# Performance work log

Measured on AMD Instinct MI355X. Metric: run time of the kernel, lower is better.

## Reference

```python
import jax, jax.numpy as jnp
import numpy as np

NUM_FIELDS = 39
_ROW, _COL = np.triu_indices(NUM_FIELDS, k=1)  # 741 pairs, matches the double loop in __init__


def setup_inputs() -> dict:
    key = jax.random.key(0)
    x = jax.random.normal(key, (16384, NUM_FIELDS, 64), dtype=jnp.float32)
    return {"x": x}


def reference(x) -> jnp.ndarray:
    # Original: p=x[:,row,:,None], q=x[:,col,None,:], pq=p@q (B,P,d,d), then sum over both d axes.
    # sum_{a,b} p_a * q_b == (sum_a p_a) * (sum_b q_b), so we fuse and never build the d x d outer.
    s = jnp.sum(x, axis=-1)                     # [B, F] per-field embedding sums
    return s[:, _ROW] * s[:, _COL]              # [B, P] with P = F*(F-1)/2 = 741
```

## Files before the change

kernel.cpp:

```cpp
#include <hip/hip_runtime.h>

#define NF 39
#define NP 741

struct PairLUT { unsigned short rc[NP]; };

constexpr PairLUT make_lut() {
    PairLUT L{};
    int p = 0;
    for (int i = 0; i < NF; ++i)
        for (int j = i + 1; j < NF; ++j) {
            L.rc[p] = (unsigned short)((i << 8) | j);
            ++p;
        }
    return L;
}

__constant__ PairLUT LUT = make_lut();

__global__ __launch_bounds__(256) void opn_kernel(const float* __restrict__ x,
                                                  float* __restrict__ out) {
    const int b   = blockIdx.x;
    const int tid = threadIdx.x;
    __shared__ float s[NF + 1];

    const int g = tid >> 4;
    const int l = tid & 15;

    const float* xb = x + (size_t)b * (NF * 64);

    #pragma unroll
    for (int base = 0; base < NF; base += 16) {
        const int f = base + g;
        float v = 0.0f;
        if (f < NF) {
            const float4 t = *reinterpret_cast<const float4*>(xb + f * 64 + l * 4);
            v = (t.x + t.y) + (t.z + t.w);
        }
        v += __shfl_xor(v, 1);
        v += __shfl_xor(v, 2);
        v += __shfl_xor(v, 4);
        v += __shfl_xor(v, 8);
        if (f < NF && l == 0) s[f] = v;
    }
    __syncthreads();

    float* ob = out + (size_t)b * NP;
    #pragma unroll
    for (int p = tid; p < NP; p += 256) {
        const unsigned int rc = LUT.rc[p];
        ob[p] = s[rc >> 8] * s[rc & 255u];
    }
}

extern "C" void kernel_launch(void* const* d_in, const int* in_sizes, int n_in,
                              void* d_out, int out_size, void* d_ws, size_t ws_size,
                              hipStream_t stream) {
    const float* x = (const float*)d_in[0];
    float* out = (float*)d_out;
    const int B = in_sizes[0] / (NF * 64);
    opn_kernel<<<B, 256, 0, stream>>>(x, out);
}
```

Before: 37.74 us.

## Assign one wavefront per batch row and drop block-wide barrier

Each 64-lane wavefront now handles a whole batch row, with four rows per 256-thread block. All ten float4 loads per lane are issued up front before the shuffle reductions, and the block-wide __syncthreads is removed because each wave reads only its own shared-memory slice. Outputs are written with nontemporal stores. The grid is B/4, which assumes B is divisible by 4 and depends on the wave having finished its LDS writes before it reads them back without a barrier.

Result: no change. 37.28 us (median of 2 runs) (-1.2%).

```diff
diff --git a/kernel.cpp b/kernel.cpp
--- a/kernel.cpp
+++ b/kernel.cpp
@@ -2,6 +2,7 @@
 
 #define NF 39
 #define NP 741
+#define N4 624
 
 struct PairLUT { unsigned short rc[NP]; };
 
@@ -20,36 +21,46 @@
 
 __global__ __launch_bounds__(256) void opn_kernel(const float* __restrict__ x,
                                                   float* __restrict__ out) {
-    const int b   = blockIdx.x;
     const int tid = threadIdx.x;
-    __shared__ float s[NF + 1];
+    const int wid = tid >> 6;
+    const int l   = tid & 63;
+    const int b   = blockIdx.x * 4 + wid;
 
-    const int g = tid >> 4;
-    const int l = tid & 15;
+    __shared__ float s[4][NF + 1];
 
-    const float* xb = x + (size_t)b * (NF * 64);
+    const float4* xb4 = reinterpret_cast<const float4*>(x) + (size_t)b * N4;
+
+    float v[10];
+    #pragma unroll
+    for (int r = 0; r < 9; ++r) {
+        const float4 t = xb4[r * 64 + l];
+        v[r] = (t.x + t.y) + (t.z + t.w);
+    }
+    {
+        float4 t = {0.f, 0.f, 0.f, 0.f};
+        if (576 + l < N4) t = xb4[576 + l];
+        v[9] = (t.x + t.y) + (t.z + t.w);
+    }
 
     #pragma unroll
-    for (int base = 0; base < NF; base += 16) {
-        const int f = base + g;
-        float v = 0.0f;
-        if (f < NF) {
-            const float4 t = *reinterpret_cast<const float4*>(xb + f * 64 + l * 4);
-            v = (t.x + t.y) + (t.z + t.w);
-        }
-        v += __shfl_xor(v, 1);
-        v += __shfl_xor(v, 2);
-        v += __shfl_xor(v, 4);
-        v += __shfl_xor(v, 8);
-        if (f < NF && l == 0) s[f] = v;
+    for (int r = 0; r < 10; ++r) {
+        float vv = v[r];
+        vv += __shfl_xor(vv, 1);
+        vv += __shfl_xor(vv, 2);
+        vv += __shfl_xor(vv, 4);
+        vv += __shfl_xor(vv, 8);
+        const int f = r * 4 + (l >> 4);
+        if ((l & 15) == 0 && f < NF) s[wid][f] = vv;
     }
-    __syncthreads();
 
     float* ob = out + (size_t)b * NP;
     #pragma unroll
-    for (int p = tid; p < NP; p += 256) {
-        const unsigned int rc = LUT.rc[p];
-        ob[p] = s[rc >> 8] * s[rc & 255u];
+    for (int k = 0; k < 12; ++k) {
+        const int p = k * 64 + l;
+        if (p < NP) {
+            const unsigned int rc = LUT.rc[p];
+            __builtin_nontemporal_store(s[wid][rc >> 8] * s[wid][rc & 255u], ob + p);
+        }
     }
 }
 
@@ -59,5 +70,5 @@
     const float* x = (const float*)d_in[0];
     float* out = (float*)d_out;
     const int B = in_sizes[0] / (NF * 64);
-    opn_kernel<<<B, 256, 0, stream>>>(x, out);
+    opn_kernel<<<B / 4, 256, 0, stream>>>(x, out);
 }
```
